# Performance work log

Hardware: AMD Instinct MI355X
Metric: run time of the kernel (lower is better)

## Reference

```python
import jax, jax.numpy as jnp
import numpy as np

B, T, C, H = 16, 2048, 1024, 64  # batch, seq (== block_size), n_embd, head_size


def setup_inputs() -> dict:
    key = jax.random.key(0)
    ks = jax.random.split(key, 4)
    s = 1.0 / np.sqrt(C)  # Linear default init scale
    return {
        "x": jax.random.normal(ks[0], (B, T, C), dtype=jnp.float32),
        "Wq": jax.random.normal(ks[1], (C, H), dtype=jnp.float32) * s,
        "bq": jnp.zeros((H,), dtype=jnp.float32),
        "Wk": jax.random.normal(ks[2], (C, H), dtype=jnp.float32) * s,
        "bk": jnp.zeros((H,), dtype=jnp.float32),
        "Wv": jax.random.normal(ks[3], (C, H), dtype=jnp.float32) * s,
        "bv": jnp.zeros((H,), dtype=jnp.float32),
    }


def reference(x, Wq, bq, Wk, bk, Wv, bv):
    # q, k, v: (B, T, H)
    q = x @ Wq + bq
    k = x @ Wk + bk
    v = x @ Wv + bv
    # scores (B, T, T); NOTE: original code has NO 1/sqrt(H) scaling
    wei = jnp.einsum("btd,bsd->bts", q, k)
    t = x.shape[1]
    causal = jnp.tril(jnp.ones((t, t), dtype=bool))
    wei = jnp.where(causal, wei, -jnp.inf)
    # NOTE: original code applies softmax over dim=1 (query axis), kept faithfully
    wei = jax.nn.softmax(wei, axis=1)
    # dropout is identity at p=0 / eval
    out = jnp.einsum("bts,bsd->btd", wei, v)  # (B, T, H)
    return out
```

## Files before the change

kernel.cpp:

```cpp
#include <hip/hip_runtime.h>
#include <hip/hip_bf16.h>
#include <math.h>

#define TT 2048
#define NB 16

typedef short short8 __attribute__((ext_vector_type(8)));
typedef float f32x4 __attribute__((ext_vector_type(4)));
typedef unsigned short us4 __attribute__((ext_vector_type(4)));

#define MFMA16(a,b,c) __builtin_amdgcn_mfma_f32_16x16x32_bf16((a),(b),(c),0,0,0)

typedef const __attribute__((address_space(1))) unsigned gas_u32;
typedef __attribute__((address_space(3))) unsigned las_u32;

__device__ __forceinline__ void gll16(const void* g, void* l) {
    __builtin_amdgcn_global_load_lds((gas_u32*)g, (las_u32*)l, 16, 0, 0);
}

__device__ __forceinline__ unsigned short bf16rn(float f) {
    unsigned u = __float_as_uint(f);
    u += 0x7FFFu + ((u >> 16) & 1u);
    return (unsigned short)(u >> 16);
}
__device__ __forceinline__ float bf16tof(unsigned short h) {
    return __uint_as_float(((unsigned)h) << 16);
}

__global__ void wprep_kernel(const float* __restrict__ Wq,
                             const float* __restrict__ Wk,
                             const float* __restrict__ Wv,
                             short* __restrict__ WT)
{
    const int m = blockIdx.x >> 6, n = blockIdx.x & 63, tid = threadIdx.x;
    const float* W = (m == 0) ? Wq : ((m == 1) ? Wk : Wv);
    const float sc = (m == 0) ? 1.4426950408889634f : 1.f;
    const int k0 = tid * 4;
    us4 hv, lv;
#pragma unroll
    for (int r = 0; r < 4; ++r) {
        float v = W[(size_t)(k0 + r) * 64 + n] * sc;
        unsigned short hh = bf16rn(v);
        hv[r] = hh;
        lv[r] = bf16rn(v - bf16tof(hh));
    }
    *(us4*)&WT[((size_t)(m * 2 + 0) * 64 + n) * 1024 + k0] = hv;
    *(us4*)&WT[((size_t)(m * 2 + 1) * 64 + n) * 1024 + k0] = lv;
}

__global__ void zero_kernel(float* __restrict__ p) {
    p[blockIdx.x * 256 + threadIdx.x] = 0.f;
}

__global__ __launch_bounds__(256, 2) void qkv_kernel(
    const float* __restrict__ x,
    const float* __restrict__ bq, const float* __restrict__ bk,
    const float* __restrict__ bv,
    const short* __restrict__ WT,
    short* __restrict__ qhl, short* __restrict__ khl, short* __restrict__ vT)
{
    __shared__ short xs[8192];
    __shared__ short ws[24576];
    const int tid = threadIdx.x;
    const int w = tid >> 6, l15 = tid & 15, g = (tid >> 4) & 3;
    const int t0 = blockIdx.x * 64;

    f32x4 acc[12];
    const f32x4 z = {0.f, 0.f, 0.f, 0.f};
#pragma unroll
    for (int i = 0; i < 12; ++i) acc[i] = z;

#pragma unroll 1
    for (int kc = 0; kc < 16; ++kc) {
#pragma unroll
        for (int p = 0; p < 12; ++p) {
            int u = tid + p * 256;
            int part = u / 1536; int r = u - part * 1536;
            int kk = r / 768;    int r2 = r - kk * 768;
            int n = r2 >> 2, g8 = r2 & 3;
            int m = n >> 6, nn = n & 63;
            const short* src = WT + (((size_t)((m * 2 + part) * 64 + nn)) << 10)
                                  + kc * 64 + kk * 32 + g8 * 8;
            gll16(src, &ws[((tid & ~63) + p * 256) * 8]);
        }
#pragma unroll
        for (int p = 0; p < 2; ++p) {
            int idx = tid + p * 256;
            int kk = idx >> 8; int rem = idx & 255;
            int row = rem >> 2, g8 = rem & 3;
            const float* xp = x + (size_t)(t0 + row) * 1024 + kc * 64 + kk * 32 + g8 * 8;
            f32x4 a = *(const f32x4*)xp;
            f32x4 b2 = *(const f32x4*)(xp + 4);
            short8 h8, l8;
#pragma unroll
            for (int j = 0; j < 4; ++j) {
                unsigned short hh = bf16rn(a[j]);
                h8[j] = (short)hh; l8[j] = (short)bf16rn(a[j] - bf16tof(hh));
                hh = bf16rn(b2[j]);
                h8[j + 4] = (short)hh; l8[j + 4] = (short)bf16rn(b2[j] - bf16tof(hh));
            }
            *(short8*)&xs[((kk * 64 + row) * 4 + g8) * 8] = h8;
            *(short8*)&xs[(((2 + kk) * 64 + row) * 4 + g8) * 8] = l8;
        }
        __syncthreads();

#pragma unroll
        for (int kk = 0; kk < 2; ++kk) {
            short8 xf[2];
#pragma unroll
            for (int part = 0; part < 2; ++part)
                xf[part] = *(const short8*)
                    &xs[(((part * 2 + kk) * 64 + w * 16 + l15) * 4 + g) * 8];
#pragma unroll
            for (int Nb = 0; Nb < 12; ++Nb) {
                short8 wh = *(const short8*)&ws[((kk * 192 + Nb * 16 + l15) * 4 + g) * 8];
                if (Nb < 8) {
                    short8 wl = *(const short8*)
                        &ws[(((2 + kk) * 192 + Nb * 16 + l15) * 4 + g) * 8];
                    acc[Nb] = MFMA16(wh, xf[0], acc[Nb]);
                    acc[Nb] = MFMA16(wh, xf[1], acc[Nb]);
                    acc[Nb] = MFMA16(wl, xf[0], acc[Nb]);
                } else {
                    acc[Nb] = MFMA16(xf[0], wh, acc[Nb]);
                }
            }
        }
        __syncthreads();
    }

    const float LOG2E = 1.4426950408889634f;
#pragma unroll
    for (int Nb = 0; Nb < 12; ++Nb) {
        f32x4 a = acc[Nb];
        if (Nb < 8) {
            const bool isq = (Nb < 4);
            const int nbase = (Nb & 3) * 16 + g * 4;
            const int trow = t0 + w * 16 + l15;
            const float* bias = isq ? bq : bk;
            us4 hv, lv;
#pragma unroll
            for (int r = 0; r < 4; ++r) {
                float v = a[r] + (isq ? bias[nbase + r] * LOG2E : bias[nbase + r]);
                unsigned short hh = bf16rn(v);
                hv[r] = hh; lv[r] = bf16rn(v - bf16tof(hh));
            }
            short* dst = (isq ? qhl : khl) + ((size_t)trow * 2) * 64 + nbase;
            *(us4*)dst = hv;
            *(us4*)(dst + 64) = lv;
        } else {
            const int d = (Nb - 8) * 16 + l15;
            const int tbase = t0 + w * 16 + g * 4;
            const float bvd = bv[d];
            us4 pk;
#pragma unroll
            for (int r = 0; r < 4; ++r) pk[r] = bf16rn(a[r] + bvd);
            const int b = tbase >> 11, ttl = tbase & 2047;
            *(us4*)&vT[((size_t)(b * 64 + d)) * 2048 + ttl] = pk;
        }
    }
}

__global__ __launch_bounds__(256, 4) void colstats_kernel(
    const short* __restrict__ qhl, const short* __restrict__ khl,
    float* __restrict__ dcol)
{
    __shared__ short kb[8192];
    __shared__ short qb[8192];
    const int tid = threadIdx.x;
    const int w = tid >> 6, l15 = tid & 15, g = (tid >> 4) & 3;
    const int sblk = blockIdx.x, tc = blockIdx.y, b = blockIdx.z;
    const int tt0 = max(sblk, tc * 8), tt1 = min(32, tc * 8 + 8);
    if (tt0 >= tt1) return;
    const int s0 = sblk * 64;
    const int sl = w * 16 + g * 4;

#pragma unroll
    for (int p = 0; p < 4; ++p) {
        int u = tid + p * 256;
        int part = u >> 9, kk = (u >> 8) & 1, row = (u >> 2) & 63, g8 = u & 3;
        gll16(khl + ((size_t)(b * TT + s0 + row) * 2 + part) * 64 + kk * 32 + g8 * 8,
              &kb[((tid & ~63) + p * 256) * 8]);
    }

    short8 kf[2][2];
    float dsl[4] = {0.f, 0.f, 0.f, 0.f};
    const f32x4 z = {0.f, 0.f, 0.f, 0.f};

#pragma unroll 1
    for (int tt = tt0; tt < tt1; ++tt) {
#pragma unroll
        for (int p = 0; p < 4; ++p) {
            int u = tid + p * 256;
            int part = u >> 9, kk = (u >> 8) & 1, row = (u >> 2) & 63, g8 = u & 3;
            gll16(qhl + ((size_t)(b * TT + tt * 64 + row) * 2 + part) * 64 + kk * 32 + g8 * 8,
                  &qb[((tid & ~63) + p * 256) * 8]);
        }
        __syncthreads();
        if (tt == tt0) {
#pragma unroll
            for (int kk = 0; kk < 2; ++kk)
#pragma unroll
                for (int part = 0; part < 2; ++part)
                    kf[kk][part] = *(const short8*)
                        &kb[(((part * 2 + kk) * 64 + w * 16 + l15) * 4 + g) * 8];
        }
#pragma unroll
        for (int tb = 0; tb < 4; ++tb) {
            f32x4 a = z;
#pragma unroll
            for (int kk = 0; kk < 2; ++kk) {
                short8 qh = *(const short8*)&qb[((kk * 64 + tb * 16 + l15) * 4 + g) * 8];
                short8 ql = *(const short8*)&qb[(((2 + kk) * 64 + tb * 16 + l15) * 4 + g) * 8];
                a = MFMA16(kf[kk][0], qh, a);
                a = MFMA16(kf[kk][0], ql, a);
                a = MFMA16(kf[kk][1], qh, a);
            }
            if (tt == sblk) {
#pragma unroll
                for (int r = 0; r < 4; ++r)
                    if (tb * 16 + l15 < sl + r) a[r] = -INFINITY;
            }
#pragma unroll
            for (int r = 0; r < 4; ++r) dsl[r] += exp2f(a[r]);
        }
        __syncthreads();
    }
#pragma unroll
    for (int r = 0; r < 4; ++r) {
        float dv = dsl[r];
        dv += __shfl_xor(dv, 1); dv += __shfl_xor(dv, 2);
        dv += __shfl_xor(dv, 4); dv += __shfl_xor(dv, 8);
        dsl[r] = dv;
    }
    if (l15 == 0) {
#pragma unroll
        for (int r = 0; r < 4; ++r)
            atomicAdd(&dcol[(size_t)b * TT + s0 + sl + r], dsl[r]);
    }
}

__global__ __launch_bounds__(256, 2) void attnout_kernel(
    const short* __restrict__ qhl, const short* __restrict__ khl,
    const short* __restrict__ vT, const float* __restrict__ dcol,
    float* __restrict__ out)
{
    __shared__ short kb[8192];
    __shared__ short vb[4096];
    __shared__ short ebA[2048];
    __shared__ short ebB[2048];
    __shared__ float cb[64];
    const int tid = threadIdx.x;
    const int w = tid >> 6, l15 = tid & 15, g = (tid >> 4) & 3;
    const int p = blockIdx.x, b = blockIdx.y;
    const int iA = p, iB = 63 - p;
    const int nA = iA >> 1, nB = iB >> 1;
    const int sl = w * 16 + g * 4;

    short8 qfA[2][2][2], qfB[2][2][2];
#pragma unroll
    for (int tb = 0; tb < 2; ++tb)
#pragma unroll
        for (int kk = 0; kk < 2; ++kk)
#pragma unroll
            for (int part = 0; part < 2; ++part) {
                qfA[tb][kk][part] = *(const short8*)
                    (qhl + ((size_t)(b * TT + iA * 32 + tb * 16 + l15) * 2 + part) * 64
                         + kk * 32 + g * 8);
                qfB[tb][kk][part] = *(const short8*)
                    (qhl + ((size_t)(b * TT + iB * 32 + tb * 16 + l15) * 2 + part) * 64
                         + kk * 32 + g * 8);
            }

    f32x4 oaccA[2], oaccB[2];
    const f32x4 z = {0.f, 0.f, 0.f, 0.f};
    oaccA[0] = z; oaccA[1] = z; oaccB[0] = z; oaccB[1] = z;

#pragma unroll 1
    for (int ss = 0; ss <= nB; ++ss) {
        const int s0 = ss * 64;
#pragma unroll
        for (int pp = 0; pp < 4; ++pp) {
            int u = tid + pp * 256;
            int part = u >> 9, kk = (u >> 8) & 1, row = (u >> 2) & 63, g8 = u & 3;
            gll16(khl + ((size_t)(b * TT + s0 + row) * 2 + part) * 64 + kk * 32 + g8 * 8,
                  &kb[((tid & ~63) + pp * 256) * 8]);
        }
#pragma unroll
        for (int pp = 0; pp < 2; ++pp) {
            int u = tid + pp * 256;
            int kgs = u >> 8, d = (u >> 2) & 63, g8 = u & 3;
            gll16(vT + ((size_t)(b * 64 + d)) * 2048 + s0 + kgs * 32 + g8 * 8,
                  &vb[((tid & ~63) + pp * 256) * 8]);
        }
        if (tid < 64) cb[tid] = log2f(dcol[(size_t)b * TT + s0 + tid]);
        __syncthreads();

        short8 kf[2][2];
#pragma unroll
        for (int kk = 0; kk < 2; ++kk)
#pragma unroll
            for (int part = 0; part < 2; ++part)
                kf[kk][part] = *(const short8*)
                    &kb[(((part * 2 + kk) * 64 + w * 16 + l15) * 4 + g) * 8];

        const f32x4 c4 = *(const f32x4*)&cb[sl];
        const bool actA = (ss <= nA);
        const int kgs = w >> 1, g8s = (w & 1) * 2 + (g >> 1), j0 = (g & 1) * 4;

#pragma unroll
        for (int tb = 0; tb < 2; ++tb) {
            f32x4 a = z;
#pragma unroll
            for (int kk = 0; kk < 2; ++kk) {
                a = MFMA16(kf[kk][0], qfB[tb][kk][0], a);
                a = MFMA16(kf[kk][0], qfB[tb][kk][1], a);
                a = MFMA16(kf[kk][1], qfB[tb][kk][0], a);
            }
            const int tg = iB * 32 + tb * 16 + l15;
            us4 pk;
#pragma unroll
            for (int r = 0; r < 4; ++r) {
                float e = (s0 + sl + r <= tg) ? exp2f(a[r] - c4[r]) : 0.f;
                pk[r] = bf16rn(e);
            }
            *(us4*)&ebB[((kgs * 32 + tb * 16 + l15) * 4 + g8s) * 8 + j0] = pk;
        }
        if (actA) {
#pragma unroll
            for (int tb = 0; tb < 2; ++tb) {
                f32x4 a = z;
#pragma unroll
                for (int kk = 0; kk < 2; ++kk) {
                    a = MFMA16(kf[kk][0], qfA[tb][kk][0], a);
                    a = MFMA16(kf[kk][0], qfA[tb][kk][1], a);
                    a = MFMA16(kf[kk][1], qfA[tb][kk][0], a);
                }
                const int tg = iA * 32 + tb * 16 + l15;
                us4 pk;
#pragma unroll
                for (int r = 0; r < 4; ++r) {
                    float e = (s0 + sl + r <= tg) ? exp2f(a[r] - c4[r]) : 0.f;
                    pk[r] = bf16rn(e);
                }
                *(us4*)&ebA[((kgs * 32 + tb * 16 + l15) * 4 + g8s) * 8 + j0] = pk;
            }
        }
        __syncthreads();

        short8 vf[2];
#pragma unroll
        for (int kg = 0; kg < 2; ++kg)
            vf[kg] = *(const short8*)&vb[((kg * 64 + w * 16 + l15) * 4 + g) * 8];
#pragma unroll
        for (int tb = 0; tb < 2; ++tb)
#pragma unroll
            for (int kg = 0; kg < 2; ++kg) {
                short8 ef = *(const short8*)&ebB[((kg * 32 + tb * 16 + l15) * 4 + g) * 8];
                oaccB[tb] = MFMA16(vf[kg], ef, oaccB[tb]);
            }
        if (actA) {
#pragma unroll
            for (int tb = 0; tb < 2; ++tb)
#pragma unroll
                for (int kg = 0; kg < 2; ++kg) {
                    short8 ef = *(const short8*)&ebA[((kg * 32 + tb * 16 + l15) * 4 + g) * 8];
                    oaccA[tb] = MFMA16(vf[kg], ef, oaccA[tb]);
                }
        }
        __syncthreads();
    }

#pragma unroll
    for (int tb = 0; tb < 2; ++tb) {
        const int tA = iA * 32 + tb * 16 + l15;
        const int tB = iB * 32 + tb * 16 + l15;
        *(f32x4*)(out + ((size_t)(b * TT + tA)) * 64 + sl) = oaccA[tb];
        *(f32x4*)(out + ((size_t)(b * TT + tB)) * 64 + sl) = oaccB[tb];
    }
}

extern "C" void kernel_launch(void* const* d_in, const int* in_sizes, int n_in,
                              void* d_out, int out_size, void* d_ws, size_t ws_size,
                              hipStream_t stream)
{
    const float* x  = (const float*)d_in[0];
    const float* Wq = (const float*)d_in[1];
    const float* bq = (const float*)d_in[2];
    const float* Wk = (const float*)d_in[3];
    const float* bk = (const float*)d_in[4];
    const float* Wv = (const float*)d_in[5];
    const float* bv = (const float*)d_in[6];

    char* wsb = (char*)d_ws;
    short* qhl = (short*)wsb;
    short* khl = (short*)(wsb + 8388608);
    short* vTb = (short*)(wsb + 16777216);
    short* WT  = (short*)(wsb + 20971520);
    float* dcol = (float*)(wsb + 21757952);

    zero_kernel<<<dim3(128), 256, 0, stream>>>(dcol);
    wprep_kernel<<<dim3(192), 256, 0, stream>>>(Wq, Wk, Wv, WT);
    qkv_kernel<<<dim3(512), 256, 0, stream>>>(x, bq, bk, bv, WT, qhl, khl, vTb);
    colstats_kernel<<<dim3(32, 4, NB), 256, 0, stream>>>(qhl, khl, dcol);
    attnout_kernel<<<dim3(32, NB), 256, 0, stream>>>(qhl, khl, vTb, dcol, (float*)d_out);
}
```

Before: 310.3 us.

## Store unnormalized probabilities in colstats and fold column normalization into V

The column-stats pass now writes the bf16 exp scores for each causal tile to a workspace buffer laid out in the MFMA operand order. A new small kernel divides V by the column sums. The output kernel then only streams the stored P tiles and the prescaled V through double-buffered LDS staging, so it no longer recomputes QK^T and exp. This trades the recompute for roughly 70 MB of extra global write and read traffic, and it rounds V/d to bf16.

```diff
diff --git a/kernel.cpp b/kernel.cpp
--- a/kernel.cpp
+++ b/kernel.cpp
@@ -25,6 +25,11 @@
 }
 __device__ __forceinline__ float bf16tof(unsigned short h) {
     return __uint_as_float(((unsigned)h) << 16);
+}
+
+__device__ __forceinline__ int strip_base(int i) {
+    int h = i >> 1;
+    return h * (h + 1) + (i & 1) * (h + 1);
 }
 
 __global__ void wprep_kernel(const float* __restrict__ Wq,
@@ -160,9 +165,9 @@
     }
 }
 
-__global__ __launch_bounds__(256, 4) void colstats_kernel(
+__global__ __launch_bounds__(256, 4) void colstatsP_kernel(
     const short* __restrict__ qhl, const short* __restrict__ khl,
-    float* __restrict__ dcol)
+    float* __restrict__ dcol, short* __restrict__ Pst)
 {
     __shared__ short kb[8192];
     __shared__ short qb[8192];
@@ -173,6 +178,7 @@
     if (tt0 >= tt1) return;
     const int s0 = sblk * 64;
     const int sl = w * 16 + g * 4;
+    const int kgs = w >> 1, g8s = (w & 1) * 2 + (g >> 1), j0 = (g & 1) * 4;
 
 #pragma unroll
     for (int p = 0; p < 4; ++p) {
@@ -220,8 +226,18 @@
                 for (int r = 0; r < 4; ++r)
                     if (tb * 16 + l15 < sl + r) a[r] = -INFINITY;
             }
-#pragma unroll
-            for (int r = 0; r < 4; ++r) dsl[r] += exp2f(a[r]);
+            us4 pk;
+#pragma unroll
+            for (int r = 0; r < 4; ++r) {
+                float p = exp2f(a[r]);
+                dsl[r] += p;
+                pk[r] = bf16rn(p);
+            }
+            const int strip = tt * 2 + (tb >> 1);
+            const int t32 = (tb & 1) * 16 + l15;
+            size_t toff = ((size_t)(b * 1056 + strip_base(strip) + sblk)) * 2048
+                        + ((kgs * 32 + t32) * 4 + g8s) * 8 + j0;
+            *(us4*)&Pst[toff] = pk;
         }
         __syncthreads();
     }
@@ -239,16 +255,32 @@
     }
 }
 
-__global__ __launch_bounds__(256, 2) void attnout_kernel(
-    const short* __restrict__ qhl, const short* __restrict__ khl,
-    const short* __restrict__ vT, const float* __restrict__ dcol,
+__global__ void vprep_kernel(const short* __restrict__ vT,
+                             const float* __restrict__ dcol,
+                             short* __restrict__ vT2)
+{
+    const int u = blockIdx.x * 256 + threadIdx.x;
+    const int s8 = u & 255, bd = u >> 8;
+    const int b = bd >> 6;
+    short8 v = *(const short8*)&vT[(size_t)bd * 2048 + s8 * 8];
+    f32x4 d0 = *(const f32x4*)&dcol[(size_t)b * TT + s8 * 8];
+    f32x4 d1 = *(const f32x4*)&dcol[(size_t)b * TT + s8 * 8 + 4];
+    short8 o;
+#pragma unroll
+    for (int j = 0; j < 4; ++j) {
+        o[j]     = (short)bf16rn(bf16tof((unsigned short)v[j])     / d0[j]);
+        o[4 + j] = (short)bf16rn(bf16tof((unsigned short)v[4 + j]) / d1[j]);
+    }
+    *(short8*)&vT2[(size_t)bd * 2048 + s8 * 8] = o;
+}
+
+__global__ __launch_bounds__(256, 4) void attnout_kernel(
+    const short* __restrict__ Pst, const short* __restrict__ vT2,
     float* __restrict__ out)
 {
-    __shared__ short kb[8192];
-    __shared__ short vb[4096];
-    __shared__ short ebA[2048];
-    __shared__ short ebB[2048];
-    __shared__ float cb[64];
+    __shared__ short vb[2][4096];
+    __shared__ short ebA[2][2048];
+    __shared__ short ebB[2][2048];
     const int tid = threadIdx.x;
     const int w = tid >> 6, l15 = tid & 15, g = (tid >> 4) & 3;
     const int p = blockIdx.x, b = blockIdx.y;
@@ -256,118 +288,59 @@
     const int nA = iA >> 1, nB = iB >> 1;
     const int sl = w * 16 + g * 4;
 
-    short8 qfA[2][2][2], qfB[2][2][2];
-#pragma unroll
-    for (int tb = 0; tb < 2; ++tb)
-#pragma unroll
-        for (int kk = 0; kk < 2; ++kk)
-#pragma unroll
-            for (int part = 0; part < 2; ++part) {
-                qfA[tb][kk][part] = *(const short8*)
-                    (qhl + ((size_t)(b * TT + iA * 32 + tb * 16 + l15) * 2 + part) * 64
-                         + kk * 32 + g * 8);
-                qfB[tb][kk][part] = *(const short8*)
-                    (qhl + ((size_t)(b * TT + iB * 32 + tb * 16 + l15) * 2 + part) * 64
-                         + kk * 32 + g * 8);
-            }
+    const short* PA = Pst + ((size_t)(b * 1056 + strip_base(iA))) * 2048;
+    const short* PB = Pst + ((size_t)(b * 1056 + strip_base(iB))) * 2048;
+    const short* vbase = vT2 + (size_t)b * 64 * 2048;
+    const int ldsu = (tid & ~63) * 8;
+
+    auto stage = [&](int ss, int buf) {
+#pragma unroll
+        for (int pp = 0; pp < 2; ++pp) {
+            int u = tid + pp * 256;
+            int kgs = u >> 8, d = (u >> 2) & 63, g8 = u & 3;
+            gll16(vbase + ((size_t)d) * 2048 + ss * 64 + kgs * 32 + g8 * 8,
+                  &vb[buf][ldsu + pp * 2048]);
+        }
+        gll16(PB + (size_t)ss * 2048 + tid * 8, &ebB[buf][ldsu]);
+        gll16(PA + (size_t)ss * 2048 + tid * 8, &ebA[buf][ldsu]);
+    };
 
     f32x4 oaccA[2], oaccB[2];
     const f32x4 z = {0.f, 0.f, 0.f, 0.f};
     oaccA[0] = z; oaccA[1] = z; oaccB[0] = z; oaccB[1] = z;
 
+    stage(0, 0);
 #pragma unroll 1
     for (int ss = 0; ss <= nB; ++ss) {
-        const int s0 = ss * 64;
-#pragma unroll
-        for (int pp = 0; pp < 4; ++pp) {
-            int u = tid + pp * 256;
-            int part = u >> 9, kk = (u >> 8) & 1, row = (u >> 2) & 63, g8 = u & 3;
-            gll16(khl + ((size_t)(b * TT + s0 + row) * 2 + part) * 64 + kk * 32 + g8 * 8,
-                  &kb[((tid & ~63) + pp * 256) * 8]);
-        }
-#pragma unroll
-        for (int pp = 0; pp < 2; ++pp) {
-            int u = tid + pp * 256;
-            int kgs = u >> 8, d = (u >> 2) & 63, g8 = u & 3;
-            gll16(vT + ((size_t)(b * 64 + d)) * 2048 + s0 + kgs * 32 + g8 * 8,
-                  &vb[((tid & ~63) + pp * 256) * 8]);
-        }
-        if (tid < 64) cb[tid] = log2f(dcol[(size_t)b * TT + s0 + tid]);
-        __syncthreads();
-
-        short8 kf[2][2];
-#pragma unroll
-        for (int kk = 0; kk < 2; ++kk)
-#pragma unroll
-            for (int part = 0; part < 2; ++part)
-                kf[kk][part] = *(const short8*)
-                    &kb[(((part * 2 + kk) * 64 + w * 16 + l15) * 4 + g) * 8];
-
-        const f32x4 c4 = *(const f32x4*)&cb[sl];
-        const bool actA = (ss <= nA);
-        const int kgs = w >> 1, g8s = (w & 1) * 2 + (g >> 1), j0 = (g & 1) * 4;
-
-#pragma unroll
-        for (int tb = 0; tb < 2; ++tb) {
-            f32x4 a = z;
-#pragma unroll
-            for (int kk = 0; kk < 2; ++kk) {
-                a = MFMA16(kf[kk][0], qfB[tb][kk][0], a);
-                a = MFMA16(kf[kk][0], qfB[tb][kk][1], a);
-                a = MFMA16(kf[kk][1], qfB[tb][kk][0], a);
-            }
-            const int tg = iB * 32 + tb * 16 + l15;
-            us4 pk;
-#pragma unroll
-            for (int r = 0; r < 4; ++r) {
-                float e = (s0 + sl + r <= tg) ? exp2f(a[r] - c4[r]) : 0.f;
-                pk[r] = bf16rn(e);
-            }
-            *(us4*)&ebB[((kgs * 32 + tb * 16 + l15) * 4 + g8s) * 8 + j0] = pk;
-        }
-        if (actA) {
-#pragma unroll
-            for (int tb = 0; tb < 2; ++tb) {
-                f32x4 a = z;
-#pragma unroll
-                for (int kk = 0; kk < 2; ++kk) {
-                    a = MFMA16(kf[kk][0], qfA[tb][kk][0], a);
-                    a = MFMA16(kf[kk][0], qfA[tb][kk][1], a);
-                    a = MFMA16(kf[kk][1], qfA[tb][kk][0], a);
-                }
-                const int tg = iA * 32 + tb * 16 + l15;
-                us4 pk;
-#pragma unroll
-                for (int r = 0; r < 4; ++r) {
-                    float e = (s0 + sl + r <= tg) ? exp2f(a[r] - c4[r]) : 0.f;
-                    pk[r] = bf16rn(e);
-                }
-                *(us4*)&ebA[((kgs * 32 + tb * 16 + l15) * 4 + g8s) * 8 + j0] = pk;
-            }
-        }
-        __syncthreads();
-
+        const int nss = (ss < nB) ? ss + 1 : nB;
+        stage(nss, (ss + 1) & 1);
+        asm volatile("s_waitcnt vmcnt(4)" ::: "memory");
+        __builtin_amdgcn_s_barrier();
+        asm volatile("" ::: "memory");
+
+        const int cb_ = ss & 1;
         short8 vf[2];
 #pragma unroll
         for (int kg = 0; kg < 2; ++kg)
-            vf[kg] = *(const short8*)&vb[((kg * 64 + w * 16 + l15) * 4 + g) * 8];
+            vf[kg] = *(const short8*)&vb[cb_][((kg * 64 + w * 16 + l15) * 4 + g) * 8];
 #pragma unroll
         for (int tb = 0; tb < 2; ++tb)
 #pragma unroll
             for (int kg = 0; kg < 2; ++kg) {
-                short8 ef = *(const short8*)&ebB[((kg * 32 + tb * 16 + l15) * 4 + g) * 8];
+                short8 ef = *(const short8*)&ebB[cb_][((kg * 32 + tb * 16 + l15) * 4 + g) * 8];
                 oaccB[tb] = MFMA16(vf[kg], ef, oaccB[tb]);
             }
-        if (actA) {
+        if (ss <= nA) {
 #pragma unroll
             for (int tb = 0; tb < 2; ++tb)
 #pragma unroll
                 for (int kg = 0; kg < 2; ++kg) {
-                    short8 ef = *(const short8*)&ebA[((kg * 32 + tb * 16 + l15) * 4 + g) * 8];
+                    short8 ef = *(const short8*)&ebA[cb_][((kg * 32 + tb * 16 + l15) * 4 + g) * 8];
                     oaccA[tb] = MFMA16(vf[kg], ef, oaccA[tb]);
                 }
         }
-        __syncthreads();
+        asm volatile("" ::: "memory");
+        __builtin_amdgcn_s_barrier();
     }
 
 #pragma unroll
@@ -392,15 +365,18 @@
     const float* bv = (const float*)d_in[6];
 
     char* wsb = (char*)d_ws;
-    short* qhl = (short*)wsb;
-    short* khl = (short*)(wsb + 8388608);
-    short* vTb = (short*)(wsb + 16777216);
-    short* WT  = (short*)(wsb + 20971520);
-    float* dcol = (float*)(wsb + 21757952);
+    short* qhl  = (short*)wsb;
+    short* khl  = (short*)(wsb + 8388608);
+    short* vTb  = (short*)(wsb + 16777216);
+    short* vT2  = (short*)(wsb + 20971520);
+    short* WT   = (short*)(wsb + 25165824);
+    float* dcol = (float*)(wsb + 25952256);
+    short* Pst  = (short*)(wsb + 26083328);
 
     zero_kernel<<<dim3(128), 256, 0, stream>>>(dcol);
     wprep_kernel<<<dim3(192), 256, 0, stream>>>(Wq, Wk, Wv, WT);
     qkv_kernel<<<dim3(512), 256, 0, stream>>>(x, bq, bk, bv, WT, qhl, khl, vTb);
-    colstats_kernel<<<dim3(32, 4, NB), 256, 0, stream>>>(qhl, khl, dcol);
-    attnout_kernel<<<dim3(32, NB), 256, 0, stream>>>(qhl, khl, vTb, dcol, (float*)d_out);
-}
+    colstatsP_kernel<<<dim3(32, 4, NB), 256, 0, stream>>>(qhl, khl, dcol, Pst);
+    vprep_kernel<<<dim3(1024), 256, 0, stream>>>(vTb, dcol, vT2);
+    attnout_kernel<<<dim3(32, NB), 256, 0, stream>>>(Pst, vT2, (float*)d_out);
+}
```

Result: faster. 295.7 us (-4.7%).
